# Kernel optimization log

Hardware: AMD Instinct MI355X
Metric: run time of the kernel (lower is better)

## Reference

```python
import jax, jax.numpy as jnp
import numpy as np

N = 100000
D = 64
E = 1600000
EPS = 1e-5


def setup_inputs() -> dict:
    key = jax.random.key(0)
    k1, k2, k3, k4, k5, k6 = jax.random.split(key, 6)
    node_features = jax.random.normal(k1, (N, D), dtype=jnp.float32)
    edge_index = jax.random.randint(k2, (E, 2), 0, N, dtype=jnp.int64)
    # torch Linear params: W [out, in], b [out]
    lim_m = 1.0 / np.sqrt(2 * D)
    W_msg = jax.random.uniform(k3, (D, 2 * D), minval=-lim_m, maxval=lim_m, dtype=jnp.float32)
    b_msg = jax.random.uniform(k4, (D,), minval=-lim_m, maxval=lim_m, dtype=jnp.float32)
    W_upd = jax.random.uniform(k5, (D, 2 * D), minval=-lim_m, maxval=lim_m, dtype=jnp.float32)
    b_upd = jax.random.uniform(k6, (D,), minval=-lim_m, maxval=lim_m, dtype=jnp.float32)
    gamma = jnp.ones((D,), dtype=jnp.float32)
    beta = jnp.zeros((D,), dtype=jnp.float32)
    return {
        "node_features": node_features,
        "edge_index": edge_index,
        "W_msg": W_msg,
        "b_msg": b_msg,
        "W_upd": W_upd,
        "b_upd": b_upd,
        "gamma": gamma,
        "beta": beta,
    }


def _layer_norm(x, gamma, beta):
    mu = jnp.mean(x, axis=-1, keepdims=True)
    var = jnp.mean(jnp.square(x - mu), axis=-1, keepdims=True)
    return (x - mu) * jax.lax.rsqrt(var + EPS) * gamma + beta


def reference(node_features, edge_index, W_msg, b_msg, W_upd, b_upd, gamma, beta):
    src = edge_index[:, 0]
    tgt = edge_index[:, 1]
    # per-edge message: relu(Linear(cat(x[src], x[tgt])))  -- split weight to avoid [E,2D] concat
    Wm_s = W_msg[:, :D]  # [D, D] applied to src feats
    Wm_t = W_msg[:, D:]  # [D, D] applied to tgt feats
    msg = jax.nn.relu(node_features[src] @ Wm_s.T + node_features[tgt] @ Wm_t.T + b_msg)  # [E, D]
    # scatter-mean into target nodes
    messages = jax.ops.segment_sum(msg, tgt, num_segments=N)  # [N, D]
    counts = jax.ops.segment_sum(jnp.ones((edge_index.shape[0],), dtype=node_features.dtype), tgt, num_segments=N)
    counts = jnp.maximum(counts, 1.0)[:, None]
    messages = messages / counts
    # update: relu(Linear(cat(x, messages))) + residual + LayerNorm
    Wu_x = W_upd[:, :D]
    Wu_m = W_upd[:, D:]
    updated = jax.nn.relu(node_features @ Wu_x.T + messages @ Wu_m.T + b_upd)
    return _layer_norm(updated + node_features, gamma, beta)
```

## Files before the change

### kernel.cpp

```cpp
#include <hip/hip_runtime.h>
#include <hip/hip_bf16.h>
#include <stdint.h>

#define NNODES 100000
#define DF 64
#define NEDGES 1600000
#define ND (NNODES * DF)
#define BKT 100
#define NBUCK 1000
#define CHUNK 128
#define NCHUNK (NEDGES / CHUNK)

static __device__ __forceinline__ float bf2f(unsigned short u) {
    union { uint32_t i; float f; } c; c.i = ((uint32_t)u) << 16; return c.f;
}
static __device__ __forceinline__ void unpack2(uint32_t u, float& lo, float& hi) {
    union { uint32_t i; float f; } a, b;
    a.i = u << 16; b.i = u & 0xFFFF0000u;
    lo = a.f; hi = b.f;
}

__global__ void detect_k(const unsigned short* __restrict__ x,
                         const unsigned int* __restrict__ ei,
                         int* __restrict__ flags) {
    __shared__ int cnt_sane, cnt_odd_nz;
    if (threadIdx.x == 0) { cnt_sane = 0; cnt_odd_nz = 0; }
    __syncthreads();
    unsigned short s = x[threadIdx.x * 2];
    unsigned short m = s & 0x7FFF;
    if (m < 0x0080 || (m >= 0x3000 && m <= 0x4200)) atomicAdd(&cnt_sane, 1);
    if (threadIdx.x < 64) {
        if (ei[threadIdx.x * 2 + 1] != 0u) atomicAdd(&cnt_odd_nz, 1);
    }
    __syncthreads();
    if (threadIdx.x == 0) {
        flags[0] = (cnt_sane >= 192) ? 1 : 0;
        flags[1] = (cnt_odd_nz == 0) ? 1 : 0;
    }
}

__global__ void wconv_k(const int* __restrict__ flags,
                        const void* __restrict__ Wm, const void* __restrict__ Wu,
                        const void* __restrict__ bm, const void* __restrict__ bu,
                        const void* __restrict__ ga, const void* __restrict__ be,
                        float* __restrict__ WfMT, float* __restrict__ WfUT,
                        float* __restrict__ prm) {
    const int bf = flags[0];
    int i = blockIdx.x * 256 + threadIdx.x;
    if (i < 16384) {
        const void* src = (i < 8192) ? Wm : Wu;
        float* dst = (i < 8192) ? WfMT : WfUT;
        int ii = i & 8191, j = ii >> 6, k = ii & 63;
        int si = (j & 63) * 128 + ((j >> 6) ? 64 : 0) + k;
        float v = bf ? bf2f(((const unsigned short*)src)[si]) : ((const float*)src)[si];
        dst[(j >> 6) * 4096 + k * 64 + (j & 63)] = v;
    } else if (i < 16384 + 320) {
        int t = i - 16384, which = t >> 6, k = t & 63;
        if (which == 4) { prm[t] = 0.f; }
        else {
            const void* p = (which == 0) ? bm : (which == 1) ? bu : (which == 2) ? ga : be;
            prm[t] = bf ? bf2f(((const unsigned short*)p)[k]) : ((const float*)p)[k];
        }
    }
}

__global__ __launch_bounds__(256, 1) void mm_k(const int* __restrict__ flags,
                                               const void* __restrict__ xv,
                                               const float* __restrict__ WT,
                                               const float* __restrict__ bias,
                                               void* __restrict__ outv,
                                               int of) {
    const int lane = threadIdx.x & 63;
    const int wib = __builtin_amdgcn_readfirstlane(threadIdx.x >> 6);
    const int bf = flags[0];

    float w[64];
    #pragma unroll
    for (int k = 0; k < 64; ++k) w[k] = WT[k * 64 + lane];
    const float bs = bias[lane];

    const int wv = blockIdx.x * 4 + wib;
    const int nw = gridDim.x * 4;
    for (int n = wv; n < NNODES; n += nw) {
        float a0 = 0.f, a1 = 0.f, a2 = 0.f, a3 = 0.f;
        if (bf) {
            const uint4* xr = (const uint4*)((const unsigned short*)xv + (size_t)n * DF);
            #pragma unroll
            for (int q = 0; q < 8; ++q) {
                uint4 v = xr[q];
                float x0,x1,x2,x3,x4,x5,x6,x7;
                unpack2(v.x, x0, x1); unpack2(v.y, x2, x3);
                unpack2(v.z, x4, x5); unpack2(v.w, x6, x7);
                a0 = fmaf(x0, w[8*q+0], a0); a1 = fmaf(x1, w[8*q+1], a1);
                a2 = fmaf(x2, w[8*q+2], a2); a3 = fmaf(x3, w[8*q+3], a3);
                a0 = fmaf(x4, w[8*q+4], a0); a1 = fmaf(x5, w[8*q+5], a1);
                a2 = fmaf(x6, w[8*q+6], a2); a3 = fmaf(x7, w[8*q+7], a3);
            }
        } else {
            const float4* xr = (const float4*)((const float*)xv + (size_t)n * DF);
            #pragma unroll
            for (int q = 0; q < 16; ++q) {
                float4 v = xr[q];
                a0 = fmaf(v.x, w[4*q+0], a0); a1 = fmaf(v.y, w[4*q+1], a1);
                a2 = fmaf(v.z, w[4*q+2], a2); a3 = fmaf(v.w, w[4*q+3], a3);
            }
        }
        float r = (a0 + a1) + (a2 + a3) + bs;
        size_t gi = (size_t)n * DF + lane;
        if (of) ((float*)outv)[gi] = r;
        else    ((__hip_bfloat16*)outv)[gi] = __float2bfloat16(r);
    }
}

__global__ __launch_bounds__(256) void bhist_k(const int* __restrict__ flags,
                                               const int* __restrict__ ei,
                                               int* __restrict__ BktCnt) {
    __shared__ int h[NBUCK];
    const int i64 = flags[1];
    for (int i = threadIdx.x; i < NBUCK; i += 256) h[i] = 0;
    __syncthreads();
    int stride = gridDim.x * 256;
    for (int e = blockIdx.x * 256 + threadIdx.x; e < NEDGES; e += stride) {
        int tgt = i64 ? ei[4*e + 2] : ei[2*e + 1];
        if ((unsigned)tgt < NNODES) atomicAdd(&h[tgt / BKT], 1);
    }
    __syncthreads();
    for (int b = threadIdx.x; b < NBUCK; b += 256)
        if (h[b]) atomicAdd(BktCnt + b, h[b]);
}

__global__ __launch_bounds__(1024) void bscan_k(const int* __restrict__ BktCnt,
                                                int* __restrict__ BktOff,
                                                int* __restrict__ BktCur) {
    __shared__ int lds[1024];
    int t = threadIdx.x;
    int c = (t < NBUCK) ? BktCnt[t] : 0;
    lds[t] = c;
    __syncthreads();
    for (int off = 1; off < 1024; off <<= 1) {
        int add = (t >= off) ? lds[t - off] : 0;
        __syncthreads();
        lds[t] += add;
        __syncthreads();
    }
    if (t < NBUCK) {
        int ex = lds[t] - c;
        BktOff[t] = ex;
        BktCur[t] = ex;
    }
    if (t == NBUCK - 1) BktOff[NBUCK] = lds[t];
}

__global__ __launch_bounds__(256) void bfill_k(const int* __restrict__ flags,
                                               const int* __restrict__ ei,
                                               int* __restrict__ BktCur,
                                               int* __restrict__ BktE) {
    __shared__ int h[NBUCK], h2[NBUCK], basee[NBUCK];
    const int i64 = flags[1];
    for (int i = threadIdx.x; i < NBUCK; i += 256) { h[i] = 0; h2[i] = 0; }
    __syncthreads();
    const int stride = gridDim.x * 256;
    for (int e = blockIdx.x * 256 + threadIdx.x; e < NEDGES; e += stride) {
        int tgt = i64 ? ei[4*e + 2] : ei[2*e + 1];
        if ((unsigned)tgt < NNODES) atomicAdd(&h[tgt / BKT], 1);
    }
    __syncthreads();
    for (int b = threadIdx.x; b < NBUCK; b += 256)
        if (h[b]) basee[b] = atomicAdd(BktCur + b, h[b]);
    __syncthreads();
    for (int e = blockIdx.x * 256 + threadIdx.x; e < NEDGES; e += stride) {
        int src, tgt;
        if (i64) { src = ei[4*e]; tgt = ei[4*e + 2]; }
        else     { src = ei[2*e]; tgt = ei[2*e + 1]; }
        if ((unsigned)tgt >= NNODES) continue;
        int b = tgt / BKT;
        int tl = tgt - b * BKT;
        int r = atomicAdd(&h2[b], 1);
        BktE[basee[b] + r] = (tl << 24) | (src & 0xFFFFFF);
    }
}

__global__ __launch_bounds__(256) void tsort_k(const int* __restrict__ BktOff,
                                               const int* __restrict__ BktE,
                                               int* __restrict__ CsrSrc,
                                               int* __restrict__ Row) {
    __shared__ int oc[128], excl[128], cur[128];
    const int tid = threadIdx.x;
    const int b = blockIdx.x;
    const int s = BktOff[b], e = BktOff[b + 1];
    const int n = e - s;
    if (tid < 128) { oc[tid] = 0; }
    __syncthreads();
    for (int i = tid; i < n; i += 256)
        atomicAdd(&oc[((unsigned)BktE[s + i]) >> 24], 1);
    __syncthreads();
    if (tid < 128) excl[tid] = (tid > 0) ? oc[tid - 1] : 0;
    __syncthreads();
    for (int off = 1; off < 128; off <<= 1) {
        int add = (tid >= off && tid < 128) ? excl[tid - off] : 0;
        __syncthreads();
        if (tid < 128) excl[tid] += add;
        __syncthreads();
    }
    if (tid < BKT) {
        Row[b * BKT + tid] = s + excl[tid];
        cur[tid] = excl[tid];
    }
    if (b == 0 && tid == 0) Row[NNODES] = NEDGES;
    __syncthreads();
    for (int i = tid; i < n; i += 256) {
        int v = BktE[s + i];
        int tl = ((unsigned)v) >> 24;
        int p = atomicAdd(&cur[tl], 1);
        CsrSrc[s + p] = v & 0xFFFFFF;
    }
}

__global__ __launch_bounds__(256) void agg_k(const __hip_bfloat16* __restrict__ Ps,
                                             const __hip_bfloat16* __restrict__ Pt,
                                             const int* __restrict__ Row,
                                             const int* __restrict__ CsrSrc,
                                             __hip_bfloat16* __restrict__ Msg) {
    const int lane = threadIdx.x & 63;
    const int wib = __builtin_amdgcn_readfirstlane(threadIdx.x >> 6);
    const int w = blockIdx.x * 4 + wib;
    if (w >= NCHUNK) return;
    const int eA = w * CHUNK;
    const int hiB = (w == NCHUNK - 1) ? (NEDGES + 1) : (eA + CHUNK);

    int lo = 0, hi = NNODES + 1;
    while (lo < hi) { int mid = (lo + hi) >> 1; if (Row[mid] >= eA) hi = mid; else lo = mid + 1; }
    const int t_lo = lo;
    lo = t_lo; hi = NNODES + 1;
    while (lo < hi) { int mid = (lo + hi) >> 1; if (Row[mid] >= hiB) hi = mid; else lo = mid + 1; }
    int t_hi = lo;
    if (t_hi > NNODES) t_hi = NNODES;

    const unsigned short* Ps16 = (const unsigned short*)Ps;
    const unsigned short* Pt16 = (const unsigned short*)Pt;

    for (int t = t_lo; t < t_hi; ++t) {
        const int segS = Row[t], segE = Row[t + 1];
        const int deg = segE - segS;
        float pt = bf2f(Pt16[(size_t)t * DF + lane]);
        float macc = 0.f;
        int i = segS;
        for (; i + 8 <= segE; i += 8) {
            int s0 = CsrSrc[i+0], s1 = CsrSrc[i+1], s2 = CsrSrc[i+2], s3 = CsrSrc[i+3];
            int s4 = CsrSrc[i+4], s5 = CsrSrc[i+5], s6 = CsrSrc[i+6], s7 = CsrSrc[i+7];
            if ((unsigned)s0 >= NNODES) s0 = 0;
            if ((unsigned)s1 >= NNODES) s1 = 0;
            if ((unsigned)s2 >= NNODES) s2 = 0;
            if ((unsigned)s3 >= NNODES) s3 = 0;
            if ((unsigned)s4 >= NNODES) s4 = 0;
            if ((unsigned)s5 >= NNODES) s5 = 0;
            if ((unsigned)s6 >= NNODES) s6 = 0;
            if ((unsigned)s7 >= NNODES) s7 = 0;
            float p0 = bf2f(Ps16[(size_t)s0 * DF + lane]);
            float p1 = bf2f(Ps16[(size_t)s1 * DF + lane]);
            float p2 = bf2f(Ps16[(size_t)s2 * DF + lane]);
            float p3 = bf2f(Ps16[(size_t)s3 * DF + lane]);
            float p4 = bf2f(Ps16[(size_t)s4 * DF + lane]);
            float p5 = bf2f(Ps16[(size_t)s5 * DF + lane]);
            float p6 = bf2f(Ps16[(size_t)s6 * DF + lane]);
            float p7 = bf2f(Ps16[(size_t)s7 * DF + lane]);
            macc += fmaxf(p0 + pt, 0.f) + fmaxf(p1 + pt, 0.f)
                  + fmaxf(p2 + pt, 0.f) + fmaxf(p3 + pt, 0.f)
                  + fmaxf(p4 + pt, 0.f) + fmaxf(p5 + pt, 0.f)
                  + fmaxf(p6 + pt, 0.f) + fmaxf(p7 + pt, 0.f);
        }
        for (; i < segE; ++i) {
            int s0 = CsrSrc[i];
            if ((unsigned)s0 >= NNODES) s0 = 0;
            macc += fmaxf(bf2f(Ps16[(size_t)s0 * DF + lane]) + pt, 0.f);
        }
        float mval = (deg > 0) ? (macc / (float)deg) : 0.f;
        Msg[(size_t)t * DF + lane] = __float2bfloat16(mval);
    }
}

__global__ __launch_bounds__(256, 1) void u2_k(const int* __restrict__ flags,
                                               const void* __restrict__ xv,
                                               const __hip_bfloat16* __restrict__ Msg,
                                               const float* __restrict__ t1,
                                               const float* __restrict__ WT,
                                               const float* __restrict__ prm,
                                               void* __restrict__ outv) {
    const int lane = threadIdx.x & 63;
    const int wib = __builtin_amdgcn_readfirstlane(threadIdx.x >> 6);
    const int bf = flags[0];

    float w[64];
    #pragma unroll
    for (int k = 0; k < 64; ++k) w[k] = WT[k * 64 + lane];
    const float ga = prm[128 + lane];
    const float be = prm[192 + lane];

    const unsigned short* x16 = (const unsigned short*)xv;
    const float* xf = (const float*)xv;

    const int wv = blockIdx.x * 4 + wib;
    const int nw = gridDim.x * 4;
    for (int n = wv; n < NNODES; n += nw) {
        float b0 = 0.f, b1 = 0.f, b2 = 0.f, b3 = 0.f;
        const uint4* mw = (const uint4*)((const unsigned short*)Msg + (size_t)n * DF);
        #pragma unroll
        for (int q = 0; q < 8; ++q) {
            uint4 v = mw[q];
            float m0,m1,m2,m3,m4,m5,m6,m7;
            unpack2(v.x, m0, m1); unpack2(v.y, m2, m3);
            unpack2(v.z, m4, m5); unpack2(v.w, m6, m7);
            b0 = fmaf(m0, w[8*q+0], b0); b1 = fmaf(m1, w[8*q+1], b1);
            b2 = fmaf(m2, w[8*q+2], b2); b3 = fmaf(m3, w[8*q+3], b3);
            b0 = fmaf(m4, w[8*q+4], b0); b1 = fmaf(m5, w[8*q+5], b1);
            b2 = fmaf(m6, w[8*q+6], b2); b3 = fmaf(m7, w[8*q+7], b3);
        }
        size_t gi = (size_t)n * DF + lane;
        float t  = t1[gi];
        float xl = bf ? bf2f(x16[gi]) : xf[gi];
        float u = fmaxf((b0 + b1) + (b2 + b3) + t, 0.f);
        float r = u + xl;

        float s = r, s2 = r * r;
        #pragma unroll
        for (int m = 1; m < 64; m <<= 1) {
            s  += __shfl_xor(s, m, 64);
            s2 += __shfl_xor(s2, m, 64);
        }
        float mu  = s * (1.0f / 64.0f);
        float var = fmaxf(s2 * (1.0f / 64.0f) - mu * mu, 0.f);
        float o = (r - mu) * rsqrtf(var + 1e-5f) * ga + be;

        if (bf) ((__hip_bfloat16*)outv)[gi] = __float2bfloat16(o);
        else    ((float*)outv)[gi] = o;
    }
}

extern "C" void kernel_launch(void* const* d_in, const int* in_sizes, int n_in,
                              void* d_out, int out_size, void* d_ws, size_t ws_size,
                              hipStream_t stream) {
    const void* x  = d_in[0];
    const int*  ei = (const int*)d_in[1];
    const void* Wm = d_in[2];
    const void* bm = d_in[3];
    const void* Wu = d_in[4];
    const void* bu = d_in[5];
    const void* ga = d_in[6];
    const void* be = d_in[7];

    char* ws = (char*)d_ws;
    size_t off = 0;
    __hip_bfloat16* Ps  = (__hip_bfloat16*)(ws + off); off += (size_t)ND * 2;
    __hip_bfloat16* Pt  = (__hip_bfloat16*)(ws + off); off += (size_t)ND * 2;
    __hip_bfloat16* Msg = (__hip_bfloat16*)(ws + off); off += (size_t)ND * 2;
    int*   BktE   = (int*)(ws + off); off += (size_t)NEDGES * 4;
    int*   CsrSrc = (int*)(ws + off); off += (size_t)NEDGES * 4;
    int*   Row    = (int*)(ws + off); off += (size_t)(NNODES + 1) * 4;
    int*   BktCnt = (int*)(ws + off); off += NBUCK * 4;
    int*   BktOff = (int*)(ws + off); off += (NBUCK + 1) * 4;
    int*   BktCur = (int*)(ws + off); off += NBUCK * 4;
    int*   flg    = (int*)(ws + off); off += 16;
    float* WfMT   = (float*)(ws + off); off += 8192 * 4;
    float* WfUT   = (float*)(ws + off); off += 8192 * 4;
    float* prm    = (float*)(ws + off); off += 320 * 4;

    float* t1 = (float*)Ps;

    (void)hipMemsetAsync(BktCnt, 0, NBUCK * 4, stream);

    detect_k<<<1, 256, 0, stream>>>((const unsigned short*)x, (const unsigned int*)ei, flg);
    wconv_k<<<65, 256, 0, stream>>>(flg, Wm, Wu, bm, bu, ga, be, WfMT, WfUT, prm);

    mm_k<<<1024, 256, 0, stream>>>(flg, x, WfMT,        prm + 256, Ps, 0);
    mm_k<<<1024, 256, 0, stream>>>(flg, x, WfMT + 4096, prm,       Pt, 0);

    bhist_k<<<256, 256, 0, stream>>>(flg, ei, BktCnt);
    bscan_k<<<1, 1024, 0, stream>>>(BktCnt, BktOff, BktCur);
    bfill_k<<<128, 256, 0, stream>>>(flg, ei, BktCur, BktE);
    tsort_k<<<NBUCK, 256, 0, stream>>>(BktOff, BktE, CsrSrc, Row);

    agg_k<<<(NCHUNK + 3) / 4, 256, 0, stream>>>(Ps, Pt, Row, CsrSrc, Msg);

    mm_k<<<1024, 256, 0, stream>>>(flg, x, WfUT, prm + 64, t1, 1);

    u2_k<<<1024, 256, 0, stream>>>(flg, x, Msg, t1, WfUT + 4096, prm, d_out);
}
```

Before: 338.8 us.

## Split projected features into four column slices for cache-local gather aggregation

Ps, Pt and Msg are stored as four 16-column slices instead of 64-wide rows. The aggregation grid is quadrupled so each block handles one slice, and each wave processes 4 edges in parallel with 16 lanes per edge, then reduces across lane groups with shuffles. Each slice is about 3.2 MB, so the gather working set per block is smaller and may fit better in cache. In exchange, the binary searches over Row and the CsrSrc reads are repeated four times, and u2_k now reads Msg from four separate slices. The wconv_k grid also grows by one block, which looks unrelated.

```diff
diff --git a/kernel.cpp b/kernel.cpp
--- a/kernel.cpp
+++ b/kernel.cpp
@@ -10,9 +10,15 @@
 #define NBUCK 1000
 #define CHUNK 128
 #define NCHUNK (NEDGES / CHUNK)
+#define NSL 4
+#define SW 16
+#define SLN ((size_t)NNODES * SW)
 
 static __device__ __forceinline__ float bf2f(unsigned short u) {
     union { uint32_t i; float f; } c; c.i = ((uint32_t)u) << 16; return c.f;
+}
+static __device__ __forceinline__ unsigned short f2bf(float f) {
+    union { __hip_bfloat16 b; unsigned short u; } c; c.b = __float2bfloat16(f); return c.u;
 }
 static __device__ __forceinline__ void unpack2(uint32_t u, float& lo, float& hi) {
     union { uint32_t i; float f; } a, b;
@@ -106,9 +112,12 @@
             }
         }
         float r = (a0 + a1) + (a2 + a3) + bs;
-        size_t gi = (size_t)n * DF + lane;
-        if (of) ((float*)outv)[gi] = r;
-        else    ((__hip_bfloat16*)outv)[gi] = __float2bfloat16(r);
+        if (of) {
+            ((float*)outv)[(size_t)n * DF + lane] = r;
+        } else {
+            size_t gi = (size_t)(lane >> 4) * SLN + (size_t)n * SW + (lane & 15);
+            ((unsigned short*)outv)[gi] = f2bf(r);
+        }
     }
 }
 
@@ -216,17 +225,26 @@
     }
 }
 
-__global__ __launch_bounds__(256) void agg_k(const __hip_bfloat16* __restrict__ Ps,
-                                             const __hip_bfloat16* __restrict__ Pt,
+__global__ __launch_bounds__(256) void agg_k(const unsigned short* __restrict__ Ps,
+                                             const unsigned short* __restrict__ Pt,
                                              const int* __restrict__ Row,
                                              const int* __restrict__ CsrSrc,
-                                             __hip_bfloat16* __restrict__ Msg) {
+                                             unsigned short* __restrict__ Msg) {
     const int lane = threadIdx.x & 63;
     const int wib = __builtin_amdgcn_readfirstlane(threadIdx.x >> 6);
-    const int w = blockIdx.x * 4 + wib;
-    if (w >= NCHUNK) return;
-    const int eA = w * CHUNK;
-    const int hiB = (w == NCHUNK - 1) ? (NEDGES + 1) : (eA + CHUNK);
+    const int sl = blockIdx.x & 3;
+    const int cb = blockIdx.x >> 2;
+    const int c = cb * 4 + wib;
+    if (c >= NCHUNK) return;
+    const int d  = lane & 15;
+    const int eg = lane >> 4;
+
+    const unsigned short* Ps_s = Ps + (size_t)sl * SLN;
+    const unsigned short* Pt_s = Pt + (size_t)sl * SLN;
+    unsigned short*       Ms_s = Msg + (size_t)sl * SLN;
+
+    const int eA = c * CHUNK;
+    const int hiB = (c == NCHUNK - 1) ? (NEDGES + 1) : (eA + CHUNK);
 
     int lo = 0, hi = NNODES + 1;
     while (lo < hi) { int mid = (lo + hi) >> 1; if (Row[mid] >= eA) hi = mid; else lo = mid + 1; }
@@ -236,52 +254,34 @@
     int t_hi = lo;
     if (t_hi > NNODES) t_hi = NNODES;
 
-    const unsigned short* Ps16 = (const unsigned short*)Ps;
-    const unsigned short* Pt16 = (const unsigned short*)Pt;
-
     for (int t = t_lo; t < t_hi; ++t) {
         const int segS = Row[t], segE = Row[t + 1];
         const int deg = segE - segS;
-        float pt = bf2f(Pt16[(size_t)t * DF + lane]);
+        float ptv = bf2f(Pt_s[(size_t)t * SW + d]);
         float macc = 0.f;
-        int i = segS;
-        for (; i + 8 <= segE; i += 8) {
-            int s0 = CsrSrc[i+0], s1 = CsrSrc[i+1], s2 = CsrSrc[i+2], s3 = CsrSrc[i+3];
-            int s4 = CsrSrc[i+4], s5 = CsrSrc[i+5], s6 = CsrSrc[i+6], s7 = CsrSrc[i+7];
-            if ((unsigned)s0 >= NNODES) s0 = 0;
-            if ((unsigned)s1 >= NNODES) s1 = 0;
-            if ((unsigned)s2 >= NNODES) s2 = 0;
-            if ((unsigned)s3 >= NNODES) s3 = 0;
-            if ((unsigned)s4 >= NNODES) s4 = 0;
-            if ((unsigned)s5 >= NNODES) s5 = 0;
-            if ((unsigned)s6 >= NNODES) s6 = 0;
-            if ((unsigned)s7 >= NNODES) s7 = 0;
-            float p0 = bf2f(Ps16[(size_t)s0 * DF + lane]);
-            float p1 = bf2f(Ps16[(size_t)s1 * DF + lane]);
-            float p2 = bf2f(Ps16[(size_t)s2 * DF + lane]);
-            float p3 = bf2f(Ps16[(size_t)s3 * DF + lane]);
-            float p4 = bf2f(Ps16[(size_t)s4 * DF + lane]);
-            float p5 = bf2f(Ps16[(size_t)s5 * DF + lane]);
-            float p6 = bf2f(Ps16[(size_t)s6 * DF + lane]);
-            float p7 = bf2f(Ps16[(size_t)s7 * DF + lane]);
-            macc += fmaxf(p0 + pt, 0.f) + fmaxf(p1 + pt, 0.f)
-                  + fmaxf(p2 + pt, 0.f) + fmaxf(p3 + pt, 0.f)
-                  + fmaxf(p4 + pt, 0.f) + fmaxf(p5 + pt, 0.f)
-                  + fmaxf(p6 + pt, 0.f) + fmaxf(p7 + pt, 0.f);
-        }
-        for (; i < segE; ++i) {
-            int s0 = CsrSrc[i];
-            if ((unsigned)s0 >= NNODES) s0 = 0;
-            macc += fmaxf(bf2f(Ps16[(size_t)s0 * DF + lane]) + pt, 0.f);
-        }
+        for (int i = segS; i < segE; i += 8) {
+            int idxA = i + eg;
+            int idxB = idxA + 4;
+            int iA = (idxA < segE) ? idxA : segS;
+            int iB = (idxB < segE) ? idxB : segS;
+            int sA = CsrSrc[iA]; if ((unsigned)sA >= NNODES) sA = 0;
+            int sB = CsrSrc[iB]; if ((unsigned)sB >= NNODES) sB = 0;
+            float pA = bf2f(Ps_s[(size_t)sA * SW + d]);
+            float pB = bf2f(Ps_s[(size_t)sB * SW + d]);
+            float vA = (idxA < segE) ? fmaxf(pA + ptv, 0.f) : 0.f;
+            float vB = (idxB < segE) ? fmaxf(pB + ptv, 0.f) : 0.f;
+            macc += vA + vB;
+        }
+        macc += __shfl_xor(macc, 16, 64);
+        macc += __shfl_xor(macc, 32, 64);
         float mval = (deg > 0) ? (macc / (float)deg) : 0.f;
-        Msg[(size_t)t * DF + lane] = __float2bfloat16(mval);
+        if (lane < 16) Ms_s[(size_t)t * SW + d] = f2bf(mval);
     }
 }
 
 __global__ __launch_bounds__(256, 1) void u2_k(const int* __restrict__ flags,
                                                const void* __restrict__ xv,
-                                               const __hip_bfloat16* __restrict__ Msg,
+                                               const unsigned short* __restrict__ Msg,
                                                const float* __restrict__ t1,
                                                const float* __restrict__ WT,
                                                const float* __restrict__ prm,
@@ -303,17 +303,21 @@
     const int nw = gridDim.x * 4;
     for (int n = wv; n < NNODES; n += nw) {
         float b0 = 0.f, b1 = 0.f, b2 = 0.f, b3 = 0.f;
-        const uint4* mw = (const uint4*)((const unsigned short*)Msg + (size_t)n * DF);
         #pragma unroll
-        for (int q = 0; q < 8; ++q) {
-            uint4 v = mw[q];
-            float m0,m1,m2,m3,m4,m5,m6,m7;
-            unpack2(v.x, m0, m1); unpack2(v.y, m2, m3);
-            unpack2(v.z, m4, m5); unpack2(v.w, m6, m7);
-            b0 = fmaf(m0, w[8*q+0], b0); b1 = fmaf(m1, w[8*q+1], b1);
-            b2 = fmaf(m2, w[8*q+2], b2); b3 = fmaf(m3, w[8*q+3], b3);
-            b0 = fmaf(m4, w[8*q+4], b0); b1 = fmaf(m5, w[8*q+5], b1);
-            b2 = fmaf(m6, w[8*q+6], b2); b3 = fmaf(m7, w[8*q+7], b3);
+        for (int s4 = 0; s4 < NSL; ++s4) {
+            const uint4* mw = (const uint4*)(Msg + (size_t)s4 * SLN + (size_t)n * SW);
+            #pragma unroll
+            for (int q = 0; q < 2; ++q) {
+                uint4 v = mw[q];
+                const int kb = s4 * 16 + q * 8;
+                float m0,m1,m2,m3,m4,m5,m6,m7;
+                unpack2(v.x, m0, m1); unpack2(v.y, m2, m3);
+                unpack2(v.z, m4, m5); unpack2(v.w, m6, m7);
+                b0 = fmaf(m0, w[kb+0], b0); b1 = fmaf(m1, w[kb+1], b1);
+                b2 = fmaf(m2, w[kb+2], b2); b3 = fmaf(m3, w[kb+3], b3);
+                b0 = fmaf(m4, w[kb+4], b0); b1 = fmaf(m5, w[kb+5], b1);
+                b2 = fmaf(m6, w[kb+6], b2); b3 = fmaf(m7, w[kb+7], b3);
+            }
         }
         size_t gi = (size_t)n * DF + lane;
         float t  = t1[gi];
@@ -350,9 +354,9 @@
 
     char* ws = (char*)d_ws;
     size_t off = 0;
-    __hip_bfloat16* Ps  = (__hip_bfloat16*)(ws + off); off += (size_t)ND * 2;
-    __hip_bfloat16* Pt  = (__hip_bfloat16*)(ws + off); off += (size_t)ND * 2;
-    __hip_bfloat16* Msg = (__hip_bfloat16*)(ws + off); off += (size_t)ND * 2;
+    unsigned short* Ps  = (unsigned short*)(ws + off); off += (size_t)ND * 2;
+    unsigned short* Pt  = (unsigned short*)(ws + off); off += (size_t)ND * 2;
+    unsigned short* Msg = (unsigned short*)(ws + off); off += (size_t)ND * 2;
     int*   BktE   = (int*)(ws + off); off += (size_t)NEDGES * 4;
     int*   CsrSrc = (int*)(ws + off); off += (size_t)NEDGES * 4;
     int*   Row    = (int*)(ws + off); off += (size_t)(NNODES + 1) * 4;
@@ -369,7 +373,7 @@
     (void)hipMemsetAsync(BktCnt, 0, NBUCK * 4, stream);
 
     detect_k<<<1, 256, 0, stream>>>((const unsigned short*)x, (const unsigned int*)ei, flg);
-    wconv_k<<<65, 256, 0, stream>>>(flg, Wm, Wu, bm, bu, ga, be, WfMT, WfUT, prm);
+    wconv_k<<<66, 256, 0, stream>>>(flg, Wm, Wu, bm, bu, ga, be, WfMT, WfUT, prm);
 
     mm_k<<<1024, 256, 0, stream>>>(flg, x, WfMT,        prm + 256, Ps, 0);
     mm_k<<<1024, 256, 0, stream>>>(flg, x, WfMT + 4096, prm,       Pt, 0);
@@ -379,7 +383,7 @@
     bfill_k<<<128, 256, 0, stream>>>(flg, ei, BktCur, BktE);
     tsort_k<<<NBUCK, 256, 0, stream>>>(BktOff, BktE, CsrSrc, Row);
 
-    agg_k<<<(NCHUNK + 3) / 4, 256, 0, stream>>>(Ps, Pt, Row, CsrSrc, Msg);
+    agg_k<<<NCHUNK, 256, 0, stream>>>(Ps, Pt, Row, CsrSrc, Msg);
 
     mm_k<<<1024, 256, 0, stream>>>(flg, x, WfUT, prm + 64, t1, 1);
 
```

After: 412.4 us. 21.7% more time.
